# Performance work log

Measured on AMD Instinct MI355X. Metric: run time of the kernel, lower is better.

The kernel has to match this reference:

```python
import jax, jax.numpy as jnp
import numpy as np


def setup_inputs() -> dict:
    key = jax.random.key(0)
    k1, k2 = jax.random.split(key)
    B, S, H, D = 4, 2048, 12, 64
    v = jax.random.normal(k1, (B, S, H, D), dtype=jnp.float32)
    # learned per-head positional weights, sorted ascending along last dim
    # (mirrors torch.sort(torch.randn(H, S), dim=-1)[0])
    w = jnp.sort(jax.random.normal(k2, (H, S), dtype=jnp.float32), axis=-1)
    return {"v": v, "w": w}


def reference(v, w):
    # PositionalBias._naive
    # v: [B, S, H, D]; w: [H, S_max]
    B, S, H, D = v.shape
    seq_len = S - 2  # v[:, 1:-1] is the non-special-token span
    w_ = w[:, :seq_len]  # [H, seq_len]
    # _construct_bias builds bias[h, l, j] = w[h, |l - j|] (symmetric Toeplitz)
    pos = jnp.arange(seq_len)
    idx = jnp.abs(pos[:, None] - pos[None, :])  # [seq_len, seq_len]
    bias = w_[:, idx]  # [H, seq_len, seq_len]
    # zero-pad one row/col on each side -> [H, S, S]
    bias = jnp.pad(bias, ((0, 0), (1, 1), (1, 1)))
    # z_pb: [1, S, H]
    z_pb = jnp.sum(bias, axis=-1).T[None, :, :]
    # pbv: [B, S, H, D]
    pbv = jnp.einsum('nlhd,hlj->njhd', v, bias)
    return (pbv, z_pb)
```

## Files before the change

kernel.cpp:

```cpp
#include <hip/hip_runtime.h>
#include <hip/hip_bf16.h>


typedef short short8 __attribute__((ext_vector_type(8)));
typedef float floatx4 __attribute__((ext_vector_type(4)));

#define TL 2280

__device__ __attribute__((aligned(16))) short g_vt[4 * 12 * 64 * 2048];

__device__ __forceinline__ unsigned short f2bf(float f) {
  union { __hip_bfloat16 b; unsigned short u; } cv;
  cv.b = __float2bfloat16(f);
  return cv.u;
}

__global__ __launch_bounds__(256) void prep_kernel(const float* __restrict__ v,
                                                   const float* __restrict__ w,
                                                   float* __restrict__ out) {
  __shared__ float zls[4096];
  __shared__ float wsum[4];

  const int bx  = blockIdx.x;
  const int tid = threadIdx.x;

  if (bx >= 384) {
    const int h = bx - 384;
    float* wvv = zls;
    float* pfx = zls + 2048;
    const float* wh = w + (size_t)h * 2048;
    float* zout = out + 6291456;
    for (int i = tid; i < 2048; i += 256) wvv[i] = (i < 2046) ? wh[i] : 0.f;
    __syncthreads();
    const int base = tid * 8;
    float run0 = 0.f;
    #pragma unroll
    for (int k = 0; k < 8; ++k) run0 += wvv[base + k];
    float x = run0;
    #pragma unroll
    for (int dd = 1; dd < 64; dd <<= 1) {
      float y = __shfl_up(x, dd);
      if ((tid & 63) >= dd) x += y;
    }
    if ((tid & 63) == 63) wsum[tid >> 6] = x;
    __syncthreads();
    const int wid4 = tid >> 6;
    float woff = 0.f;
    #pragma unroll
    for (int u = 0; u < 3; ++u) { float t = wsum[u]; if (u < wid4) woff += t; }
    float pr = x + woff - run0;
    #pragma unroll
    for (int k = 0; k < 8; ++k) { pr += wvv[base + k]; pfx[base + k] = pr; }
    __syncthreads();
    for (int i = tid; i < 2046; i += 256) {
      float z = pfx[i] + pfx[2045 - i] - wvv[0];
      zout[(size_t)(i + 1) * 12 + h] = z;
    }
    if (tid == 0) { zout[h] = 0.f; zout[(size_t)2047 * 12 + h] = 0.f; }
    return;
  }

  const int chunk = bx & 7;
  const int slice = bx >> 3;
  const int n = slice / 12, h = slice - n * 12;
  const int lane = tid & 63;
  const int wv   = tid >> 6;
  const int l0 = chunk * 256 + wv * 64;

  const float* src = v + (((size_t)n * 2048 + l0) * 12 + h) * 64 + lane;
  short* dst = g_vt + (((size_t)n * 12 + h) * 64 + lane) * 2048 + l0;

  #pragma unroll
  for (int k = 0; k < 8; ++k) {
    float f[8];
    #pragma unroll
    for (int i = 0; i < 8; ++i) f[i] = src[(size_t)(k * 8 + i) * 768];
    short8 b;
    #pragma unroll
    for (int i = 0; i < 8; ++i) {
      int l = l0 + k * 8 + i;
      b[i] = (l == 0 || l == 2047) ? (short)0 : (short)f2bf(f[i]);
    }
    *(short8*)&dst[k * 8] = b;
  }
}

__global__ __launch_bounds__(256, 3) void gemm_kernel(const float* __restrict__ w,
                                                      float* __restrict__ out) {
  __shared__ __attribute__((aligned(16))) short Tls[8 * TL];

  const int bx  = blockIdx.x;
  const int tid = threadIdx.x;

  const int slice = bx % 48;
  const int jt    = bx / 48;
  const int ndt = slice & 3;
  const int h   = slice >> 2;
  const int lane = tid & 63, wid = tid >> 6;
  const int lm = lane & 15, quad = lane >> 4;
  const int jb = jt * 128;
  const int d  = wid * 16 + lm;

  const short* vtb = g_vt + (((size_t)ndt * 12 + h) * 64 + d) * 2048;

  short8 bc0 = *(const short8*)&vtb[quad * 8];
  short8 bc1 = *(const short8*)&vtb[32 + quad * 8];

  const float* wh = w + (size_t)h * 2048;
  for (int g = tid; g < 8 * (TL / 8); g += 256) {
    int c  = g / (TL / 8);
    int p8 = (g - c * (TL / 8)) * 8;
    unsigned short buf[8] __attribute__((aligned(16)));
    #pragma unroll
    for (int i = 0; i < 8; ++i) {
      int t = 127 + jb - (p8 + i) - c;
      int a = t < 0 ? -t : t;
      buf[i] = (a <= 2045) ? f2bf(wh[a]) : (unsigned short)0;
    }
    *(short8*)&Tls[c * TL + p8] = *(const short8*)buf;
  }
  __syncthreads();

  const int pbase = 127 + quad * 8 - lm;
  auto load_af = [&](int p0) -> short8 {
    int c = p0 & 7;
    return *(const short8*)&Tls[c * TL + (p0 - c)];
  };

  short8 afr[10];
  #pragma unroll
  for (int i = 0; i < 10; ++i) afr[i] = load_af((i - 7) * 16 + pbase);

  floatx4 acc[8];
  #pragma unroll
  for (int ma = 0; ma < 8; ++ma) acc[ma] = (floatx4){0.f, 0.f, 0.f, 0.f};

  #pragma unroll 4
  for (int t = 0; t < 32; ++t) {
    const int l0 = t * 64;
    const int lb = ((t < 31) ? (t + 1) : 31) * 64 + quad * 8;
    short8 bn0 = *(const short8*)&vtb[lb];
    short8 bn1 = *(const short8*)&vtb[lb + 32];
    const int l0n = (t < 31) ? l0 + 64 : l0;
    short8 na0 = load_af(l0n - 16 + pbase);
    short8 na1 = load_af(l0n      + pbase);
    short8 na2 = load_af(l0n + 16 + pbase);
    short8 na3 = load_af(l0n + 32 + pbase);

    #pragma unroll
    for (int ma = 0; ma < 8; ++ma)
      acc[ma] = __builtin_amdgcn_mfma_f32_16x16x32_bf16(afr[7 - ma], bc0, acc[ma], 0, 0, 0);
    #pragma unroll
    for (int ma = 0; ma < 8; ++ma)
      acc[ma] = __builtin_amdgcn_mfma_f32_16x16x32_bf16(afr[9 - ma], bc1, acc[ma], 0, 0, 0);

    bc0 = bn0; bc1 = bn1;
    #pragma unroll
    for (int i = 0; i < 6; ++i) afr[i] = afr[i + 4];
    afr[6] = na0; afr[7] = na1; afr[8] = na2; afr[9] = na3;
  }

  float* obase = out + (size_t)ndt * 1572864 + (size_t)h * 64 + d;
  #pragma unroll
  for (int ma = 0; ma < 8; ++ma) {
    floatx4 cc = acc[ma];
    #pragma unroll
    for (int r = 0; r < 4; ++r) {
      int j = jb + ma * 16 + quad * 4 + r;
      float val = (j == 0 || j == 2047) ? 0.f : cc[r];
      obase[(size_t)j * 768] = val;
    }
  }
}

extern "C" void kernel_launch(void* const* d_in, const int* in_sizes, int n_in,
                              void* d_out, int out_size, void* d_ws, size_t ws_size,
                              hipStream_t stream) {
  const float* v = (const float*)d_in[0];
  const float* w = (const float*)d_in[1];
  float* out = (float*)d_out;
  prep_kernel<<<dim3(396), 256, 0, stream>>>(v, w, out);
  gemm_kernel<<<dim3(768), 256, 0, stream>>>(w, out);
}
```

Measured before the change: 129.7 us.

## Precompute global Toeplitz A-fragments in prep and stream them from global memory

New measurement: 128.4 us. About the same (-1.0%).

```diff
diff --git a/kernel.cpp b/kernel.cpp
--- a/kernel.cpp
+++ b/kernel.cpp
@@ -5,9 +5,10 @@
 typedef short short8 __attribute__((ext_vector_type(8)));
 typedef float floatx4 __attribute__((ext_vector_type(4)));
 
-#define TL 2280
+#define QN 4288
 
 __device__ __attribute__((aligned(16))) short g_vt[4 * 12 * 64 * 2048];
+__device__ __attribute__((aligned(16))) short g_wt[12 * QN * 8];
 
 __device__ __forceinline__ unsigned short f2bf(float f) {
   union { __hip_bfloat16 b; unsigned short u; } cv;
@@ -23,6 +24,23 @@
 
   const int bx  = blockIdx.x;
   const int tid = threadIdx.x;
+
+  if (bx >= 396) {
+    const int h = bx - 396;
+    const float* wh = w + (size_t)h * 2048;
+    short* F = g_wt + (size_t)h * QN * 8;
+    for (int q = tid; q < QN; q += 256) {
+      unsigned short buf[8] __attribute__((aligned(16)));
+      #pragma unroll
+      for (int i = 0; i < 8; ++i) {
+        int t = 2174 - q - i;
+        int a = t < 0 ? -t : t;
+        buf[i] = (a <= 2045) ? f2bf(wh[a]) : (unsigned short)0;
+      }
+      *(short8*)&F[(size_t)q * 8] = *(const short8*)buf;
+    }
+    return;
+  }
 
   if (bx >= 384) {
     const int h = bx - 384;
@@ -85,10 +103,7 @@
   }
 }
 
-__global__ __launch_bounds__(256, 3) void gemm_kernel(const float* __restrict__ w,
-                                                      float* __restrict__ out) {
-  __shared__ __attribute__((aligned(16))) short Tls[8 * TL];
-
+__global__ __launch_bounds__(256, 3) void gemm_kernel(float* __restrict__ out) {
   const int bx  = blockIdx.x;
   const int tid = threadIdx.x;
 
@@ -96,68 +111,68 @@
   const int jt    = bx / 48;
   const int ndt = slice & 3;
   const int h   = slice >> 2;
-  const int lane = tid & 63, wid = tid >> 6;
+  const int lane = tid & 63;
+  const int wid  = tid >> 6;
   const int lm = lane & 15, quad = lane >> 4;
   const int jb = jt * 128;
   const int d  = wid * 16 + lm;
 
   const short* vtb = g_vt + (((size_t)ndt * 12 + h) * 64 + d) * 2048;
+  const short* wtb = g_wt + (size_t)h * QN * 8;
+  const int lane_base = 127 + quad * 8 - lm + 2047 - jb;
 
-  short8 bc0 = *(const short8*)&vtb[quad * 8];
-  short8 bc1 = *(const short8*)&vtb[32 + quad * 8];
-
-  const float* wh = w + (size_t)h * 2048;
-  for (int g = tid; g < 8 * (TL / 8); g += 256) {
-    int c  = g / (TL / 8);
-    int p8 = (g - c * (TL / 8)) * 8;
-    unsigned short buf[8] __attribute__((aligned(16)));
-    #pragma unroll
-    for (int i = 0; i < 8; ++i) {
-      int t = 127 + jb - (p8 + i) - c;
-      int a = t < 0 ? -t : t;
-      buf[i] = (a <= 2045) ? f2bf(wh[a]) : (unsigned short)0;
-    }
-    *(short8*)&Tls[c * TL + p8] = *(const short8*)buf;
-  }
-  __syncthreads();
-
-  const int pbase = 127 + quad * 8 - lm;
-  auto load_af = [&](int p0) -> short8 {
-    int c = p0 & 7;
-    return *(const short8*)&Tls[c * TL + (p0 - c)];
+  auto load_af = [&](int q) -> short8 {
+    return *(const short8*)&wtb[(size_t)q << 3];
+  };
+  auto load_bf = [&](int lb) -> short8 {
+    return *(const short8*)&vtb[lb];
   };
 
   short8 afr[10];
   #pragma unroll
-  for (int i = 0; i < 10; ++i) afr[i] = load_af((i - 7) * 16 + pbase);
+  for (int i = 0; i < 10; ++i) afr[i] = load_af((i - 7) * 16 + lane_base);
+  short8 bc0 = load_bf(quad * 8);
+  short8 bc1 = load_bf(32 + quad * 8);
+  short8 bn0 = load_bf(64 + quad * 8);
+  short8 bn1 = load_bf(96 + quad * 8);
 
   floatx4 acc[8];
   #pragma unroll
   for (int ma = 0; ma < 8; ++ma) acc[ma] = (floatx4){0.f, 0.f, 0.f, 0.f};
 
-  #pragma unroll 4
+  #pragma unroll
   for (int t = 0; t < 32; ++t) {
-    const int l0 = t * 64;
-    const int lb = ((t < 31) ? (t + 1) : 31) * 64 + quad * 8;
-    short8 bn0 = *(const short8*)&vtb[lb];
-    short8 bn1 = *(const short8*)&vtb[lb + 32];
-    const int l0n = (t < 31) ? l0 + 64 : l0;
-    short8 na0 = load_af(l0n - 16 + pbase);
-    short8 na1 = load_af(l0n      + pbase);
-    short8 na2 = load_af(l0n + 16 + pbase);
-    short8 na3 = load_af(l0n + 32 + pbase);
+    short8 bm0, bm1;
+    if (t < 30) {
+      const int lb = (t + 2) * 64 + quad * 8;
+      bm0 = load_bf(lb);
+      bm1 = load_bf(lb + 32);
+    }
+    short8 na0, na1, na2, na3;
+    if (t < 31) {
+      const int l0n = t * 64 + 64;
+      na0 = load_af(l0n - 16 + lane_base);
+      na1 = load_af(l0n      + lane_base);
+      na2 = load_af(l0n + 16 + lane_base);
+      na3 = load_af(l0n + 32 + lane_base);
+    }
 
+    __builtin_amdgcn_s_setprio(1);
     #pragma unroll
     for (int ma = 0; ma < 8; ++ma)
       acc[ma] = __builtin_amdgcn_mfma_f32_16x16x32_bf16(afr[7 - ma], bc0, acc[ma], 0, 0, 0);
     #pragma unroll
     for (int ma = 0; ma < 8; ++ma)
       acc[ma] = __builtin_amdgcn_mfma_f32_16x16x32_bf16(afr[9 - ma], bc1, acc[ma], 0, 0, 0);
+    __builtin_amdgcn_s_setprio(0);
 
-    bc0 = bn0; bc1 = bn1;
-    #pragma unroll
-    for (int i = 0; i < 6; ++i) afr[i] = afr[i + 4];
-    afr[6] = na0; afr[7] = na1; afr[8] = na2; afr[9] = na3;
+    if (t < 31) {
+      #pragma unroll
+      for (int i = 0; i < 6; ++i) afr[i] = afr[i + 4];
+      afr[6] = na0; afr[7] = na1; afr[8] = na2; afr[9] = na3;
+      bc0 = bn0; bc1 = bn1;
+      if (t < 30) { bn0 = bm0; bn1 = bm1; }
+    }
   }
 
   float* obase = out + (size_t)ndt * 1572864 + (size_t)h * 64 + d;
@@ -179,6 +194,6 @@
   const float* v = (const float*)d_in[0];
   const float* w = (const float*)d_in[1];
   float* out = (float*)d_out;
-  prep_kernel<<<dim3(396), 256, 0, stream>>>(v, w, out);
-  gemm_kernel<<<dim3(768), 256, 0, stream>>>(w, out);
+  prep_kernel<<<dim3(408), 256, 0, stream>>>(v, w, out);
+  gemm_kernel<<<dim3(768), 256, 0, stream>>>(out);
 }
```
